# Performance work log

Hardware: AMD Instinct MI355X
Metric: run time of the kernel (lower is better)

## Reference

```python
import jax, jax.numpy as jnp
import numpy as np


def setup_inputs() -> dict:
    key = jax.random.key(0)
    ks = jax.random.split(key, 8)
    N0, D0, E0 = 100000, 25000, 600000   # block0: src, dst, edges
    N1, D1, E1 = 25000, 5000, 120000     # block1: src, dst, edges
    IN, HID, OUT = 128, 128, 64
    h = jax.random.normal(ks[0], (N0, IN), dtype=jnp.float32)
    src0 = jax.random.randint(ks[1], (E0,), 0, N0)
    dst0 = jax.random.randint(ks[2], (E0,), 0, D0)
    src1 = jax.random.randint(ks[3], (E1,), 0, N1)
    dst1 = jax.random.randint(ks[4], (E1,), 0, D1)
    W1 = jax.random.normal(ks[5], (IN, HID), dtype=jnp.float32) / np.float32(np.sqrt(IN))
    b1 = jnp.zeros((HID,), dtype=jnp.float32)
    W2 = jax.random.normal(ks[6], (HID, OUT), dtype=jnp.float32) / np.float32(np.sqrt(HID))
    b2 = jnp.zeros((OUT,), dtype=jnp.float32)
    return dict(h=h, W1=W1, b1=b1, W2=W2, b2=b2,
                src0=src0, dst0=dst0, src1=src1, dst1=dst1,
                num_dst0=D0, num_dst1=D1)


def reference(h, W1, b1, W2, b2, src0, dst0, src1, dst1, num_dst0, num_dst1):
    # Layer 0: copy_u + sum aggregation (gather src feats, segment-sum to dst), then Linear+ReLU.
    y0 = jax.ops.segment_sum(h[src0], dst0, num_segments=num_dst0)   # [D0, IN]
    h1 = jax.nn.relu(y0 @ W1 + b1)                                   # [D0, HID]; dropout is identity at eval
    # Layer 1 (final): aggregation then Linear, no activation.
    y1 = jax.ops.segment_sum(h1[src1], dst1, num_segments=num_dst1)  # [D1, HID]
    return y1 @ W2 + b2                                              # [D1, OUT]
```

## Files before the change

kernel.cpp:

```cpp
#include <hip/hip_runtime.h>
#include <hip/hip_bf16.h>


#define D0_CONST 25000
#define D1_CONST 5000
#define LCAP 64
#define OVFB 64
#define RGN_CAP 4096
#define NRANGE 236
#define GD1OFF 25088

typedef __attribute__((ext_vector_type(8))) short bf16x8;
typedef __attribute__((ext_vector_type(4))) float f32x4;
typedef __attribute__((ext_vector_type(4))) float f32x4v;
typedef __attribute__((ext_vector_type(4))) unsigned int u32x4;

__device__ __forceinline__ unsigned short f2bf(float f) {
    __hip_bfloat16 b = __float2bfloat16(f);
    return *(unsigned short*)&b;
}
__device__ __forceinline__ int swzi(int row, int e) {
    return row * 128 + (e ^ ((row & 7) << 3));
}
__device__ __forceinline__ void acc8(float* a, uint4 v) {
    a[0] += __uint_as_float(v.x << 16);
    a[1] += __uint_as_float(v.x & 0xffff0000u);
    a[2] += __uint_as_float(v.y << 16);
    a[3] += __uint_as_float(v.y & 0xffff0000u);
    a[4] += __uint_as_float(v.z << 16);
    a[5] += __uint_as_float(v.z & 0xffff0000u);
    a[6] += __uint_as_float(v.w << 16);
    a[7] += __uint_as_float(v.w & 0xffff0000u);
}
__device__ __forceinline__ f32x4v ntload_f4(const float* p) {
    return __builtin_nontemporal_load((const f32x4v*)p);
}
__device__ __forceinline__ void ntstore_u4(unsigned int* p, u32x4 v) {
    __builtin_nontemporal_store(v, (u32x4*)p);
}

__global__ __launch_bounds__(256) void prep_pack(
    const int* __restrict__ dst0, const int* __restrict__ dst1,
    unsigned short* __restrict__ gdp,
    const float* __restrict__ W1, const float* __restrict__ W2,
    unsigned short* __restrict__ W1T, unsigned short* __restrict__ W2T,
    int* __restrict__ rangecur,
    int n0, int n1)
{
    int i = blockIdx.x * 256 + threadIdx.x;
    if (i < n0) {
        int4 a = ((const int4*)dst0)[i * 2];
        int4 b = ((const int4*)dst0)[i * 2 + 1];
        u32x4 o;
        o.x = (unsigned)a.x | ((unsigned)a.y << 16);
        o.y = (unsigned)a.z | ((unsigned)a.w << 16);
        o.z = (unsigned)b.x | ((unsigned)b.y << 16);
        o.w = (unsigned)b.z | ((unsigned)b.w << 16);
        ((u32x4*)gdp)[i] = o;
    } else if (i < n0 + n1) {
        int j = i - n0;
        int4 a = ((const int4*)dst1)[j * 2];
        int4 b = ((const int4*)dst1)[j * 2 + 1];
        u32x4 o;
        o.x = (unsigned)(a.x + GD1OFF) | ((unsigned)(a.y + GD1OFF) << 16);
        o.y = (unsigned)(a.z + GD1OFF) | ((unsigned)(a.w + GD1OFF) << 16);
        o.z = (unsigned)(b.x + GD1OFF) | ((unsigned)(b.y + GD1OFF) << 16);
        o.w = (unsigned)(b.z + GD1OFF) | ((unsigned)(b.w + GD1OFF) << 16);
        ((u32x4*)gdp)[i] = o;
    } else {
        int j = i - n0 - n1;
        if (j < 128 * 128) {
            int k = j >> 7, n = j & 127;
            W1T[n * 128 + k] = f2bf(W1[j]);
        } else if (j < 128 * 128 + 128 * 64) {
            int j2 = j - 128 * 128;
            int k = j2 >> 6, n = j2 & 63;
            W2T[n * 128 + k] = f2bf(W2[j2]);
        } else {
            int k2 = j - 128 * 128 - 128 * 64;
            if (k2 < NRANGE) rangecur[k2] = k2 * RGN_CAP;
        }
    }
}

__global__ __launch_bounds__(256) void scatter_cast(
    const unsigned short* __restrict__ gdp,
    const int* __restrict__ src0, const int* __restrict__ src1,
    int E0, int ET,
    int* __restrict__ rgn, int* __restrict__ rangecur,
    const float* __restrict__ hf, unsigned int* __restrict__ hbf, int n8,
    int nbScat)
{
    __shared__ int hist[512];
    __shared__ int base[512];

    int b = blockIdx.x, t = threadIdx.x;
    if (b < nbScat) {
        hist[t] = 0; hist[t + 256] = 0;
        __syncthreads();

        int eb = b * 4096 + t * 16;
        const u32x4* gv = (const u32x4*)gdp;
        u32x4 p0 = gv[(size_t)b * 512 + t * 2];
        u32x4 p1 = gv[(size_t)b * 512 + t * 2 + 1];
        unsigned wa[8] = {p0.x, p0.y, p0.z, p0.w, p1.x, p1.y, p1.z, p1.w};
        int g[16], rk[16], dl[16];
        #pragma unroll
        for (int k = 0; k < 16; ++k) {
            unsigned gd = (wa[k >> 1] >> ((k & 1) * 16)) & 0xffffu;
            g[k]  = (int)(gd >> 7);
            dl[k] = (int)(gd & 127u);
            rk[k] = (eb + k < ET) ? atomicAdd(&hist[g[k]], 1) : 0;
        }
        __syncthreads();
        if (t < NRANGE) {
            int c = hist[t];
            base[t] = c ? atomicAdd(&rangecur[t], c) : 0;
        }
        __syncthreads();

        int s[16];
        if (eb + 16 <= E0) {
            #pragma unroll
            for (int q = 0; q < 4; ++q) {
                int4 v = ((const int4*)(src0 + eb))[q];
                s[q * 4] = v.x; s[q * 4 + 1] = v.y; s[q * 4 + 2] = v.z; s[q * 4 + 3] = v.w;
            }
        } else if (eb >= E0 && eb + 16 <= ET) {
            const int* sp = src1 + (eb - E0);
            #pragma unroll
            for (int q = 0; q < 4; ++q) {
                int4 v = ((const int4*)sp)[q];
                s[q * 4] = v.x; s[q * 4 + 1] = v.y; s[q * 4 + 2] = v.z; s[q * 4 + 3] = v.w;
            }
        } else {
            #pragma unroll
            for (int k = 0; k < 16; ++k) {
                int e = eb + k;
                s[k] = (e < E0) ? src0[e] : ((e < ET) ? src1[e - E0] : 0);
            }
        }

        #pragma unroll
        for (int k = 0; k < 16; ++k) {
            int e = eb + k;
            if (e < ET) {
                int pos = base[g[k]] + rk[k];
                if (pos < (g[k] + 1) * RGN_CAP)
                    rgn[pos] = (dl[k] << 17) | s[k];
            }
        }
    } else {
        int i = (b - nbScat) * 256 + t;
        if (i < n8) {
            f32x4v a = ntload_f4(hf + (size_t)i * 8);
            f32x4v c = ntload_f4(hf + (size_t)i * 8 + 4);
            u32x4 o;
            o.x = f2bf(a.x) | ((unsigned)f2bf(a.y) << 16);
            o.y = f2bf(a.z) | ((unsigned)f2bf(a.w) << 16);
            o.z = f2bf(c.x) | ((unsigned)f2bf(c.y) << 16);
            o.w = f2bf(c.z) | ((unsigned)f2bf(c.w) << 16);
            ntstore_u4(hbf + (size_t)i * 4, o);
        }
    }
}

__global__ __launch_bounds__(256) void gather0_linear(
    const uint4* __restrict__ x,
    const int* __restrict__ rgn, const int* __restrict__ rangecur,
    const unsigned short* __restrict__ W1T,
    const unsigned short* __restrict__ W2T,
    const float* __restrict__ b1,
    unsigned short* __restrict__ t,
    int M)
{
    __shared__ int lists[32 * LCAP];
    __shared__ int lcnt[32];
    __shared__ int lovf[OVFB];
    __shared__ int lovfc;
    __shared__ unsigned short Ys[32 * 128];
    __shared__ unsigned short H1s[32 * 128];

    int b = blockIdx.x, tid = threadIdx.x;
    int row0 = b * 32;
    int g = row0 >> 7;
    int sub = (row0 >> 5) & 3;

    if (tid < 32) lcnt[tid] = 0;
    if (tid == 0) lovfc = 0;
    __syncthreads();

    int n = rangecur[g] - g * RGN_CAP;
    if (n > RGN_CAP) n = RGN_CAP;
    const int* rp = rgn + (size_t)g * RGN_CAP;
    for (int i = tid; i < n; i += 256) {
        int e = rp[i];
        if ((e >> 22) == sub) {
            int dl = (e >> 17) & 31;
            int s  = e & 0x1FFFF;
            int r = atomicAdd(&lcnt[dl], 1);
            if (r < LCAP) lists[(dl << 6) + r] = s;
            else {
                int p2 = atomicAdd(&lovfc, 1);
                if (p2 < OVFB) lovf[p2] = (dl << 17) | s;
            }
        }
    }
    __syncthreads();

    {
        int lrow = tid >> 3, c = tid & 7;
        int nn = lcnt[lrow]; if (nn > LCAP) nn = LCAP;
        const int* lp = &lists[lrow << 6];
        float a[16];
        #pragma unroll
        for (int q = 0; q < 16; ++q) a[q] = 0.f;

        int i = 0;
        for (; i + 4 <= nn; i += 4) {
            int4 s4 = *(const int4*)&lp[i];
            uint4 v0a = x[(size_t)s4.x * 16 + c * 2];
            uint4 v0b = x[(size_t)s4.x * 16 + c * 2 + 1];
            uint4 v1a = x[(size_t)s4.y * 16 + c * 2];
            uint4 v1b = x[(size_t)s4.y * 16 + c * 2 + 1];
            uint4 v2a = x[(size_t)s4.z * 16 + c * 2];
            uint4 v2b = x[(size_t)s4.z * 16 + c * 2 + 1];
            uint4 v3a = x[(size_t)s4.w * 16 + c * 2];
            uint4 v3b = x[(size_t)s4.w * 16 + c * 2 + 1];
            acc8(a, v0a); acc8(a + 8, v0b);
            acc8(a, v1a); acc8(a + 8, v1b);
            acc8(a, v2a); acc8(a + 8, v2b);
            acc8(a, v3a); acc8(a + 8, v3b);
        }
        for (; i < nn; ++i) {
            int s0 = lp[i];
            acc8(a,     x[(size_t)s0 * 16 + c * 2]);
            acc8(a + 8, x[(size_t)s0 * 16 + c * 2 + 1]);
        }
        int no = lovfc; if (no > OVFB) no = OVFB;
        for (int k2 = 0; k2 < no; ++k2) {
            int e = lovf[k2];
            if ((e >> 17) == lrow) {
                int s0 = e & 0x1FFFF;
                acc8(a,     x[(size_t)s0 * 16 + c * 2]);
                acc8(a + 8, x[(size_t)s0 * 16 + c * 2 + 1]);
            }
        }
        uint4 o0, o1;
        o0.x = f2bf(a[0])  | ((unsigned)f2bf(a[1])  << 16);
        o0.y = f2bf(a[2])  | ((unsigned)f2bf(a[3])  << 16);
        o0.z = f2bf(a[4])  | ((unsigned)f2bf(a[5])  << 16);
        o0.w = f2bf(a[6])  | ((unsigned)f2bf(a[7])  << 16);
        o1.x = f2bf(a[8])  | ((unsigned)f2bf(a[9])  << 16);
        o1.y = f2bf(a[10]) | ((unsigned)f2bf(a[11]) << 16);
        o1.z = f2bf(a[12]) | ((unsigned)f2bf(a[13]) << 16);
        o1.w = f2bf(a[14]) | ((unsigned)f2bf(a[15]) << 16);
        *(uint4*)&Ys[swzi(lrow, c * 16)]     = o0;
        *(uint4*)&Ys[swzi(lrow, c * 16 + 8)] = o1;
    }
    __syncthreads();

    int w = tid >> 6, lane = tid & 63;
    int lr = lane & 15, lhi = lane >> 4;

    bf16x8 a1[2][4];
    #pragma unroll
    for (int m = 0; m < 2; ++m)
        #pragma unroll
        for (int kt = 0; kt < 4; ++kt)
            a1[m][kt] = *(bf16x8*)&Ys[swzi(16 * m + lr, kt * 32 + lhi * 8)];

    f32x4 acc1[2][2];
    #pragma unroll
    for (int m = 0; m < 2; ++m)
        #pragma unroll
        for (int j = 0; j < 2; ++j) acc1[m][j] = (f32x4)(0.f);

    #pragma unroll
    for (int j = 0; j < 2; ++j) {
        int ct = 2 * w + j;
        #pragma unroll
        for (int kt = 0; kt < 4; ++kt) {
            bf16x8 bb = *(const bf16x8*)&W1T[(ct * 16 + lr) * 128 + kt * 32 + lhi * 8];
            acc1[0][j] = __builtin_amdgcn_mfma_f32_16x16x32_bf16(a1[0][kt], bb, acc1[0][j], 0, 0, 0);
            acc1[1][j] = __builtin_amdgcn_mfma_f32_16x16x32_bf16(a1[1][kt], bb, acc1[1][j], 0, 0, 0);
        }
    }

    #pragma unroll
    for (int j = 0; j < 2; ++j) {
        int ct = 2 * w + j;
        float bv = b1[ct * 16 + lr];
        #pragma unroll
        for (int m = 0; m < 2; ++m)
            #pragma unroll
            for (int q = 0; q < 4; ++q) {
                float v = fmaxf(acc1[m][j][q] + bv, 0.f);
                H1s[swzi(16 * m + lhi * 4 + q, ct * 16 + lr)] = f2bf(v);
            }
    }
    __syncthreads();

    bf16x8 a2[2][4];
    #pragma unroll
    for (int m = 0; m < 2; ++m)
        #pragma unroll
        for (int kt = 0; kt < 4; ++kt)
            a2[m][kt] = *(bf16x8*)&H1s[swzi(16 * m + lr, kt * 32 + lhi * 8)];

    f32x4 acc2[2];
    acc2[0] = (f32x4)(0.f); acc2[1] = (f32x4)(0.f);
    #pragma unroll
    for (int kt = 0; kt < 4; ++kt) {
        bf16x8 bb = *(const bf16x8*)&W2T[(w * 16 + lr) * 128 + kt * 32 + lhi * 8];
        acc2[0] = __builtin_amdgcn_mfma_f32_16x16x32_bf16(a2[0][kt], bb, acc2[0], 0, 0, 0);
        acc2[1] = __builtin_amdgcn_mfma_f32_16x16x32_bf16(a2[1][kt], bb, acc2[1], 0, 0, 0);
    }

    #pragma unroll
    for (int m = 0; m < 2; ++m)
        #pragma unroll
        for (int q = 0; q < 4; ++q) {
            int row = row0 + 16 * m + lhi * 4 + q;
            if (row < M) t[(size_t)row * 64 + w * 16 + lr] = f2bf(acc2[m][q]);
        }
}

__global__ __launch_bounds__(256) void gather1_kernel(
    const uint4* __restrict__ x,
    const int* __restrict__ rgn, const int* __restrict__ rangecur,
    const float* __restrict__ b2,
    float4* __restrict__ out,
    int D)
{
    __shared__ int lists[32 * LCAP];
    __shared__ int lcnt[32];
    __shared__ int lovf[OVFB];
    __shared__ int lovfc;

    int b = blockIdx.x, tid = threadIdx.x;
    int row0 = b * 32;
    int g = 196 + (row0 >> 7);
    int sub = (row0 >> 5) & 3;

    if (tid < 32) lcnt[tid] = 0;
    if (tid == 0) lovfc = 0;
    __syncthreads();

    int n = rangecur[g] - g * RGN_CAP;
    if (n > RGN_CAP) n = RGN_CAP;
    const int* rp = rgn + (size_t)g * RGN_CAP;
    for (int i = tid; i < n; i += 256) {
        int e = rp[i];
        if ((e >> 22) == sub) {
            int dl = (e >> 17) & 31;
            int s  = e & 0x1FFFF;
            int r = atomicAdd(&lcnt[dl], 1);
            if (r < LCAP) lists[(dl << 6) + r] = s;
            else {
                int p2 = atomicAdd(&lovfc, 1);
                if (p2 < OVFB) lovf[p2] = (dl << 17) | s;
            }
        }
    }
    __syncthreads();

    int lrow = tid >> 3, c = tid & 7;
    int d = row0 + lrow;
    if (d >= D) return;
    int nn = lcnt[lrow]; if (nn > LCAP) nn = LCAP;
    const int* lp = &lists[lrow << 6];

    float a[8] = {0.f, 0.f, 0.f, 0.f, 0.f, 0.f, 0.f, 0.f};
    int i = 0;
    for (; i + 4 <= nn; i += 4) {
        int4 s4 = *(const int4*)&lp[i];
        uint4 v0 = x[(size_t)s4.x * 8 + c];
        uint4 v1 = x[(size_t)s4.y * 8 + c];
        uint4 v2 = x[(size_t)s4.z * 8 + c];
        uint4 v3 = x[(size_t)s4.w * 8 + c];
        acc8(a, v0); acc8(a, v1); acc8(a, v2); acc8(a, v3);
    }
    for (; i < nn; ++i) acc8(a, x[(size_t)lp[i] * 8 + c]);
    int no = lovfc; if (no > OVFB) no = OVFB;
    for (int k2 = 0; k2 < no; ++k2) {
        int e = lovf[k2];
        if ((e >> 17) == lrow) acc8(a, x[(size_t)(e & 0x1FFFF) * 8 + c]);
    }

    float4 blo = *(const float4*)&b2[c * 8];
    float4 bhi = *(const float4*)&b2[c * 8 + 4];
    float4 o0 = make_float4(a[0] + blo.x, a[1] + blo.y, a[2] + blo.z, a[3] + blo.w);
    float4 o1 = make_float4(a[4] + bhi.x, a[5] + bhi.y, a[6] + bhi.z, a[7] + bhi.w);
    out[(size_t)d * 16 + c * 2]     = o0;
    out[(size_t)d * 16 + c * 2 + 1] = o1;
}

extern "C" void kernel_launch(void* const* d_in, const int* in_sizes, int n_in,
                              void* d_out, int out_size, void* d_ws, size_t ws_size,
                              hipStream_t stream) {
    const float* h    = (const float*)d_in[0];
    const float* W1   = (const float*)d_in[1];
    const float* b1   = (const float*)d_in[2];
    const float* W2   = (const float*)d_in[3];
    const float* b2   = (const float*)d_in[4];
    const int*   src0 = (const int*)d_in[5];
    const int*   dst0 = (const int*)d_in[6];
    const int*   src1 = (const int*)d_in[7];
    const int*   dst1 = (const int*)d_in[8];

    const int N0 = in_sizes[0] / 128;
    const int E0 = in_sizes[5];
    const int E1 = in_sizes[7];
    const int ET = E0 + E1;
    const int D0 = D0_CONST;
    const int D1 = D1_CONST;
    const int nbScat = (ET + 4095) / 4096;

    char* p = (char*)d_ws;
    unsigned short* hbf  = (unsigned short*)p; p += (size_t)N0 * 128 * 2;
    unsigned short* tbf  = (unsigned short*)p; p += (size_t)D0 * 64 * 2;
    unsigned short* W1T  = (unsigned short*)p; p += 128 * 128 * 2;
    unsigned short* W2T  = (unsigned short*)p; p += 64 * 128 * 2;
    unsigned short* gdp  = (unsigned short*)p; p += (size_t)nbScat * 4096 * 2;
    int* rgn      = (int*)p; p += (size_t)NRANGE * RGN_CAP * 4;
    int* rangecur = (int*)p; p += 256 * 4;

    float* out = (float*)d_out;

    {
        int n0 = E0 / 8, n1 = E1 / 8;
        int tot = n0 + n1 + 128 * 128 + 128 * 64 + NRANGE;
        prep_pack<<<(tot + 255) / 256, 256, 0, stream>>>(
            dst0, dst1, gdp, W1, W2, W1T, W2T, rangecur, n0, n1);
    }

    {
        int n8 = N0 * 128 / 8;
        int castBlocks = (n8 + 255) / 256;
        scatter_cast<<<nbScat + castBlocks, 256, 0, stream>>>(
            gdp, src0, src1, E0, ET, rgn, rangecur,
            h, (unsigned int*)hbf, n8, nbScat);
    }

    {
        int blocks = (D0 + 31) / 32;
        gather0_linear<<<blocks, 256, 0, stream>>>(
            (const uint4*)hbf, rgn, rangecur, W1T, W2T, b1, tbf, D0);
    }

    {
        int blocks = (D1 + 31) / 32;
        gather1_kernel<<<blocks, 256, 0, stream>>>(
            (const uint4*)tbf, rgn, rangecur, b2, (float4*)out, D1);
    }
}
```

Measured before the change: 75.13 us.

## Fuse dst packing into scatter kernel and replace prep launch with memset

```diff
diff --git a/kernel.cpp b/kernel.cpp
--- a/kernel.cpp
+++ b/kernel.cpp
@@ -8,7 +8,6 @@
 #define OVFB 64
 #define RGN_CAP 4096
 #define NRANGE 236
-#define GD1OFF 25088
 
 typedef __attribute__((ext_vector_type(8))) short bf16x8;
 typedef __attribute__((ext_vector_type(4))) float f32x4;
@@ -39,36 +38,77 @@
     __builtin_nontemporal_store(v, (u32x4*)p);
 }
 
-__global__ __launch_bounds__(256) void prep_pack(
-    const int* __restrict__ dst0, const int* __restrict__ dst1,
-    unsigned short* __restrict__ gdp,
+__global__ __launch_bounds__(256) void scatter_cast(
+    const int* __restrict__ dst0, const int* __restrict__ src0,
+    const int* __restrict__ dst1, const int* __restrict__ src1,
+    int E0, int ET,
+    int* __restrict__ rgn, int* __restrict__ rangecur,
     const float* __restrict__ W1, const float* __restrict__ W2,
     unsigned short* __restrict__ W1T, unsigned short* __restrict__ W2T,
-    int* __restrict__ rangecur,
-    int n0, int n1)
+    const float* __restrict__ hf, unsigned int* __restrict__ hbf, int n8,
+    int nbScat, int nbW)
 {
-    int i = blockIdx.x * 256 + threadIdx.x;
-    if (i < n0) {
-        int4 a = ((const int4*)dst0)[i * 2];
-        int4 b = ((const int4*)dst0)[i * 2 + 1];
-        u32x4 o;
-        o.x = (unsigned)a.x | ((unsigned)a.y << 16);
-        o.y = (unsigned)a.z | ((unsigned)a.w << 16);
-        o.z = (unsigned)b.x | ((unsigned)b.y << 16);
-        o.w = (unsigned)b.z | ((unsigned)b.w << 16);
-        ((u32x4*)gdp)[i] = o;
-    } else if (i < n0 + n1) {
-        int j = i - n0;
-        int4 a = ((const int4*)dst1)[j * 2];
-        int4 b = ((const int4*)dst1)[j * 2 + 1];
-        u32x4 o;
-        o.x = (unsigned)(a.x + GD1OFF) | ((unsigned)(a.y + GD1OFF) << 16);
-        o.y = (unsigned)(a.z + GD1OFF) | ((unsigned)(a.w + GD1OFF) << 16);
-        o.z = (unsigned)(b.x + GD1OFF) | ((unsigned)(b.y + GD1OFF) << 16);
-        o.w = (unsigned)(b.z + GD1OFF) | ((unsigned)(b.w + GD1OFF) << 16);
-        ((u32x4*)gdp)[i] = o;
-    } else {
-        int j = i - n0 - n1;
+    __shared__ int hist[256];
+    __shared__ int base[256];
+
+    int b = blockIdx.x, t = threadIdx.x;
+    if (b < nbScat) {
+        hist[t] = 0;
+        __syncthreads();
+
+        int eb = b * 4096 + t * 16;
+        bool valid = eb < ET;
+        int dv[16], g[16], dl[16], rk[16], s[16];
+
+        if (valid) {
+            const int4* dp;
+            const int4* sp;
+            int goff;
+            if (eb < E0) {
+                dp = (const int4*)(dst0 + eb);
+                sp = (const int4*)(src0 + eb);
+                goff = 0;
+            } else {
+                dp = (const int4*)(dst1 + (eb - E0));
+                sp = (const int4*)(src1 + (eb - E0));
+                goff = 196;
+            }
+            #pragma unroll
+            for (int q = 0; q < 4; ++q) {
+                int4 v = dp[q];
+                dv[q * 4] = v.x; dv[q * 4 + 1] = v.y;
+                dv[q * 4 + 2] = v.z; dv[q * 4 + 3] = v.w;
+            }
+            #pragma unroll
+            for (int k = 0; k < 16; ++k) {
+                g[k]  = goff + (dv[k] >> 7);
+                dl[k] = dv[k] & 127;
+                rk[k] = atomicAdd(&hist[g[k]], 1);
+            }
+            #pragma unroll
+            for (int q = 0; q < 4; ++q) {
+                int4 v = sp[q];
+                s[q * 4] = v.x; s[q * 4 + 1] = v.y;
+                s[q * 4 + 2] = v.z; s[q * 4 + 3] = v.w;
+            }
+        }
+        __syncthreads();
+        if (t < NRANGE) {
+            int c = hist[t];
+            base[t] = c ? atomicAdd(&rangecur[t], c) : 0;
+        }
+        __syncthreads();
+
+        if (valid) {
+            #pragma unroll
+            for (int k = 0; k < 16; ++k) {
+                int posr = base[g[k]] + rk[k];
+                if (posr < RGN_CAP)
+                    rgn[(size_t)g[k] * RGN_CAP + posr] = (dl[k] << 17) | s[k];
+            }
+        }
+    } else if (b < nbScat + nbW) {
+        int j = (b - nbScat) * 256 + t;
         if (j < 128 * 128) {
             int k = j >> 7, n = j & 127;
             W1T[n * 128 + k] = f2bf(W1[j]);
@@ -76,82 +116,9 @@
             int j2 = j - 128 * 128;
             int k = j2 >> 6, n = j2 & 63;
             W2T[n * 128 + k] = f2bf(W2[j2]);
-        } else {
-            int k2 = j - 128 * 128 - 128 * 64;
-            if (k2 < NRANGE) rangecur[k2] = k2 * RGN_CAP;
-        }
-    }
-}
-
-__global__ __launch_bounds__(256) void scatter_cast(
-    const unsigned short* __restrict__ gdp,
-    const int* __restrict__ src0, const int* __restrict__ src1,
-    int E0, int ET,
-    int* __restrict__ rgn, int* __restrict__ rangecur,
-    const float* __restrict__ hf, unsigned int* __restrict__ hbf, int n8,
-    int nbScat)
-{
-    __shared__ int hist[512];
-    __shared__ int base[512];
-
-    int b = blockIdx.x, t = threadIdx.x;
-    if (b < nbScat) {
-        hist[t] = 0; hist[t + 256] = 0;
-        __syncthreads();
-
-        int eb = b * 4096 + t * 16;
-        const u32x4* gv = (const u32x4*)gdp;
-        u32x4 p0 = gv[(size_t)b * 512 + t * 2];
-        u32x4 p1 = gv[(size_t)b * 512 + t * 2 + 1];
-        unsigned wa[8] = {p0.x, p0.y, p0.z, p0.w, p1.x, p1.y, p1.z, p1.w};
-        int g[16], rk[16], dl[16];
-        #pragma unroll
-        for (int k = 0; k < 16; ++k) {
-            unsigned gd = (wa[k >> 1] >> ((k & 1) * 16)) & 0xffffu;
-            g[k]  = (int)(gd >> 7);
-            dl[k] = (int)(gd & 127u);
-            rk[k] = (eb + k < ET) ? atomicAdd(&hist[g[k]], 1) : 0;
-        }
-        __syncthreads();
-        if (t < NRANGE) {
-            int c = hist[t];
-            base[t] = c ? atomicAdd(&rangecur[t], c) : 0;
-        }
-        __syncthreads();
-
-        int s[16];
-        if (eb + 16 <= E0) {
-            #pragma unroll
-            for (int q = 0; q < 4; ++q) {
-                int4 v = ((const int4*)(src0 + eb))[q];
-                s[q * 4] = v.x; s[q * 4 + 1] = v.y; s[q * 4 + 2] = v.z; s[q * 4 + 3] = v.w;
-            }
-        } else if (eb >= E0 && eb + 16 <= ET) {
-            const int* sp = src1 + (eb - E0);
-            #pragma unroll
-            for (int q = 0; q < 4; ++q) {
-                int4 v = ((const int4*)sp)[q];
-                s[q * 4] = v.x; s[q * 4 + 1] = v.y; s[q * 4 + 2] = v.z; s[q * 4 + 3] = v.w;
-            }
-        } else {
-            #pragma unroll
-            for (int k = 0; k < 16; ++k) {
-                int e = eb + k;
-                s[k] = (e < E0) ? src0[e] : ((e < ET) ? src1[e - E0] : 0);
-            }
-        }
-
-        #pragma unroll
-        for (int k = 0; k < 16; ++k) {
-            int e = eb + k;
-            if (e < ET) {
-                int pos = base[g[k]] + rk[k];
-                if (pos < (g[k] + 1) * RGN_CAP)
-                    rgn[pos] = (dl[k] << 17) | s[k];
-            }
         }
     } else {
-        int i = (b - nbScat) * 256 + t;
+        int i = (b - nbScat - nbW) * 256 + t;
         if (i < n8) {
             f32x4v a = ntload_f4(hf + (size_t)i * 8);
             f32x4v c = ntload_f4(hf + (size_t)i * 8 + 4);
@@ -179,7 +146,6 @@
     __shared__ int lovf[OVFB];
     __shared__ int lovfc;
     __shared__ unsigned short Ys[32 * 128];
-    __shared__ unsigned short H1s[32 * 128];
 
     int b = blockIdx.x, tid = threadIdx.x;
     int row0 = b * 32;
@@ -190,7 +156,7 @@
     if (tid == 0) lovfc = 0;
     __syncthreads();
 
-    int n = rangecur[g] - g * RGN_CAP;
+    int n = rangecur[g];
     if (n > RGN_CAP) n = RGN_CAP;
     const int* rp = rgn + (size_t)g * RGN_CAP;
     for (int i = tid; i < n; i += 256) {
@@ -269,6 +235,7 @@
         #pragma unroll
         for (int kt = 0; kt < 4; ++kt)
             a1[m][kt] = *(bf16x8*)&Ys[swzi(16 * m + lr, kt * 32 + lhi * 8)];
+    __syncthreads();
 
     f32x4 acc1[2][2];
     #pragma unroll
@@ -296,7 +263,7 @@
             #pragma unroll
             for (int q = 0; q < 4; ++q) {
                 float v = fmaxf(acc1[m][j][q] + bv, 0.f);
-                H1s[swzi(16 * m + lhi * 4 + q, ct * 16 + lr)] = f2bf(v);
+                Ys[swzi(16 * m + lhi * 4 + q, ct * 16 + lr)] = f2bf(v);
             }
     }
     __syncthreads();
@@ -306,7 +273,7 @@
     for (int m = 0; m < 2; ++m)
         #pragma unroll
         for (int kt = 0; kt < 4; ++kt)
-            a2[m][kt] = *(bf16x8*)&H1s[swzi(16 * m + lr, kt * 32 + lhi * 8)];
+            a2[m][kt] = *(bf16x8*)&Ys[swzi(16 * m + lr, kt * 32 + lhi * 8)];
 
     f32x4 acc2[2];
     acc2[0] = (f32x4)(0.f); acc2[1] = (f32x4)(0.f);
@@ -347,7 +314,7 @@
     if (tid == 0) lovfc = 0;
     __syncthreads();
 
-    int n = rangecur[g] - g * RGN_CAP;
+    int n = rangecur[g];
     if (n > RGN_CAP) n = RGN_CAP;
     const int* rp = rgn + (size_t)g * RGN_CAP;
     for (int i = tid; i < n; i += 256) {
@@ -416,31 +383,26 @@
     const int D0 = D0_CONST;
     const int D1 = D1_CONST;
     const int nbScat = (ET + 4095) / 4096;
+    const int nbW = (128 * 128 + 128 * 64 + 255) / 256;
 
     char* p = (char*)d_ws;
-    unsigned short* hbf  = (unsigned short*)p; p += (size_t)N0 * 128 * 2;
-    unsigned short* tbf  = (unsigned short*)p; p += (size_t)D0 * 64 * 2;
-    unsigned short* W1T  = (unsigned short*)p; p += 128 * 128 * 2;
-    unsigned short* W2T  = (unsigned short*)p; p += 64 * 128 * 2;
-    unsigned short* gdp  = (unsigned short*)p; p += (size_t)nbScat * 4096 * 2;
+    unsigned short* hbf = (unsigned short*)p; p += (size_t)N0 * 128 * 2;
+    unsigned short* tbf = (unsigned short*)p; p += (size_t)D0 * 64 * 2;
+    unsigned short* W1T = (unsigned short*)p; p += 128 * 128 * 2;
+    unsigned short* W2T = (unsigned short*)p; p += 64 * 128 * 2;
     int* rgn      = (int*)p; p += (size_t)NRANGE * RGN_CAP * 4;
     int* rangecur = (int*)p; p += 256 * 4;
 
     float* out = (float*)d_out;
 
-    {
-        int n0 = E0 / 8, n1 = E1 / 8;
-        int tot = n0 + n1 + 128 * 128 + 128 * 64 + NRANGE;
-        prep_pack<<<(tot + 255) / 256, 256, 0, stream>>>(
-            dst0, dst1, gdp, W1, W2, W1T, W2T, rangecur, n0, n1);
-    }
+    hipMemsetAsync(rangecur, 0, NRANGE * sizeof(int), stream);
 
     {
         int n8 = N0 * 128 / 8;
         int castBlocks = (n8 + 255) / 256;
-        scatter_cast<<<nbScat + castBlocks, 256, 0, stream>>>(
-            gdp, src0, src1, E0, ET, rgn, rangecur,
-            h, (unsigned int*)hbf, n8, nbScat);
+        scatter_cast<<<nbScat + nbW + castBlocks, 256, 0, stream>>>(
+            dst0, src0, dst1, src1, E0, ET, rgn, rangecur,
+            W1, W2, W1T, W2T, h, (unsigned int*)hbf, n8, nbScat, nbW);
     }
 
     {
```

Result: no change. 75.80 us (+0.9%).
